# Kernel tuning notes

Measured on AMD Instinct MI355X. Metric: run time of the kernel, lower is better.

Reference implementation:

```python
import jax, jax.numpy as jnp
import numpy as np

N_NODES = 100000


def graph_conv(x, edge_index, w_rel, w_root, b):
    # PyG GraphConv with aggr='add':
    # out_i = W_root @ x_i + W_rel @ (sum_{j in N(i)} x_j) + b
    src, dst = edge_index[0], edge_index[1]
    agg = jax.ops.segment_sum(x[src], dst, num_segments=x.shape[0])  # [N, F_in]
    return x @ w_root.T + agg @ w_rel.T + b


def setup_inputs() -> dict:
    key = jax.random.key(0)
    k = jax.random.split(key, 8)
    c_in, c_hid, c_out = 128, 64, 16
    x = jax.random.normal(k[0], (N_NODES, c_in), dtype=jnp.float32)
    edge_index = jax.random.randint(k[1], (2, 640000), 0, N_NODES, dtype=jnp.int64)
    s1 = 1.0 / np.sqrt(c_in)
    s2 = 1.0 / np.sqrt(c_hid)
    return {
        "x": x,
        "edge_index": edge_index,
        "w1_rel": jax.random.uniform(k[2], (c_hid, c_in), jnp.float32, -s1, s1),
        "w1_root": jax.random.uniform(k[3], (c_hid, c_in), jnp.float32, -s1, s1),
        "b1": jax.random.uniform(k[4], (c_hid,), jnp.float32, -s1, s1),
        "w2_rel": jax.random.uniform(k[5], (c_out, c_hid), jnp.float32, -s2, s2),
        "w2_root": jax.random.uniform(k[6], (c_out, c_hid), jnp.float32, -s2, s2),
        "b2": jax.random.uniform(k[7], (c_out,), jnp.float32, -s2, s2),
    }


def reference(x, edge_index, w1_rel, w1_root, b1, w2_rel, w2_root, b2):
    h = graph_conv(x, edge_index, w1_rel, w1_root, b1)
    h = jax.nn.relu(h)
    # dropout is identity in eval mode (deterministic reference)
    h = graph_conv(h, edge_index, w2_rel, w2_root, b2)
    return jax.nn.log_softmax(h, axis=1)
```

## Files before the change

kernel.cpp:

```cpp
#include <hip/hip_runtime.h>
#include <math.h>

constexpr int CIN = 128, CHID = 64, COUT = 16;

__global__ void detect_kernel(const int* __restrict__ e, int* __restrict__ flag) {
    int v = e[2 * threadIdx.x + 1];
    unsigned long long b = __ballot(v == 0);
    if (threadIdx.x == 0) flag[0] = (b == 0xFFFFFFFFFFFFFFFFULL) ? 1 : 0;
}

__global__ void convert_hist(const int* __restrict__ e, int E,
                             const int* __restrict__ flag,
                             int* __restrict__ srcI, int* __restrict__ dstI,
                             int* __restrict__ counts) {
    int is64 = flag[0];
    int stride = gridDim.x * blockDim.x;
    for (int t = blockIdx.x * blockDim.x + threadIdx.x; t < E; t += stride) {
        int s, d;
        if (is64) { s = e[2 * t]; d = e[2 * (E + t)]; }
        else      { s = e[t];     d = e[E + t];       }
        srcI[t] = s;
        dstI[t] = d;
        atomicAdd(&counts[d], 1);
    }
}

__global__ __launch_bounds__(256)
void scan_partials(const int* __restrict__ counts, int N, int* __restrict__ blocksum) {
    __shared__ int red[256];
    const int tid = threadIdx.x;
    const int base = blockIdx.x * 1024 + tid * 4;
    int s = 0;
#pragma unroll
    for (int i = 0; i < 4; ++i) {
        int idx = base + i;
        if (idx < N) s += counts[idx];
    }
    red[tid] = s;
    __syncthreads();
    for (int d = 128; d > 0; d >>= 1) {
        if (tid < d) red[tid] += red[tid + d];
        __syncthreads();
    }
    if (tid == 0) blocksum[blockIdx.x] = red[0];
}

__global__ __launch_bounds__(1024)
void scan_blocksums(const int* __restrict__ blocksum, int NB, int* __restrict__ blockoff) {
    __shared__ int part[1024];
    const int tid = threadIdx.x;
    part[tid] = (tid < NB) ? blocksum[tid] : 0;
    __syncthreads();
    for (int d = 1; d < 1024; d <<= 1) {
        int v = (tid >= d) ? part[tid - d] : 0;
        __syncthreads();
        part[tid] += v;
        __syncthreads();
    }
    if (tid < NB) blockoff[tid] = (tid == 0) ? 0 : part[tid - 1];
}

__global__ __launch_bounds__(256)
void scan_apply(const int* __restrict__ counts, int N, const int* __restrict__ blockoff,
                int* __restrict__ rowptr, int* __restrict__ cursor) {
    __shared__ int part[256];
    const int tid = threadIdx.x;
    const int base = blockIdx.x * 1024 + tid * 4;
    int c[4];
    int s = 0;
#pragma unroll
    for (int i = 0; i < 4; ++i) {
        int idx = base + i;
        c[i] = (idx < N) ? counts[idx] : 0;
        s += c[i];
    }
    part[tid] = s;
    __syncthreads();
    for (int d = 1; d < 256; d <<= 1) {
        int v = (tid >= d) ? part[tid - d] : 0;
        __syncthreads();
        part[tid] += v;
        __syncthreads();
    }
    int prefix = blockoff[blockIdx.x] + ((tid == 0) ? 0 : part[tid - 1]);
#pragma unroll
    for (int i = 0; i < 4; ++i) {
        int idx = base + i;
        if (idx < N) {
            rowptr[idx] = prefix;
            cursor[idx] = prefix;
            prefix += c[i];
            if (idx == N - 1) rowptr[N] = prefix;
        }
    }
}

__global__ void fill_kernel(const int* __restrict__ srcI, const int* __restrict__ dstI,
                            int E, int* __restrict__ cursor, int* __restrict__ edgesrc) {
    int stride = gridDim.x * blockDim.x;
    for (int t = blockIdx.x * blockDim.x + threadIdx.x; t < E; t += stride) {
        int p = atomicAdd(&cursor[dstI[t]], 1);
        edgesrc[p] = srcI[t];
    }
}

template<int K, int KT, int OH, int NSLOT, int MBLK>
__global__ __launch_bounds__(256)
void gemm_dual48(const float* __restrict__ X, int N,
                 const float* __restrict__ Wa, const float* __restrict__ Wb,
                 const float* __restrict__ bias,
                 float* __restrict__ Da, float* __restrict__ Db) {
    constexpr int O = 2 * OH;
    constexpr int OG = OH / 4;
    constexpr int TILE = NSLOT * MBLK;
    constexpr int BLOCK = OG * NSLOT;
    constexpr int PADKT = KT + 4;
    static_assert(BLOCK == 256, "block size mismatch");

    __shared__ float wT[KT * O];
    __shared__ float xs[TILE * PADKT + (TILE / 8) * 4];
    const int tid = threadIdx.x;

    const int og = tid % OG;
    const int slot = tid / OG;
    const int o4 = og * 4;
    const float4 bv = *(const float4*)&bias[o4];

    const int n0 = blockIdx.x * TILE;
    const int node0 = slot * MBLK;
    const int xbase = node0 * PADKT + (node0 >> 3) * 4;

    float4 accA[MBLK], accB[MBLK];
#pragma unroll
    for (int i = 0; i < MBLK; ++i) {
        accA[i] = make_float4(0.f, 0.f, 0.f, 0.f);
        accB[i] = make_float4(0.f, 0.f, 0.f, 0.f);
    }

    for (int kt = 0; kt < K; kt += KT) {
        for (int i4 = tid; i4 < OH * (KT / 4); i4 += BLOCK) {
            int o = i4 % OH, kq = i4 / OH;
            float4 v = *(const float4*)&Wa[o * K + kt + kq * 4];
            wT[(4 * kq + 0) * O + o] = v.x;
            wT[(4 * kq + 1) * O + o] = v.y;
            wT[(4 * kq + 2) * O + o] = v.z;
            wT[(4 * kq + 3) * O + o] = v.w;
        }
        for (int i4 = tid; i4 < OH * (KT / 4); i4 += BLOCK) {
            int o = i4 % OH, kq = i4 / OH;
            float4 v = *(const float4*)&Wb[o * K + kt + kq * 4];
            wT[(4 * kq + 0) * O + OH + o] = v.x;
            wT[(4 * kq + 1) * O + OH + o] = v.y;
            wT[(4 * kq + 2) * O + OH + o] = v.z;
            wT[(4 * kq + 3) * O + OH + o] = v.w;
        }
        for (int i4 = tid; i4 < TILE * (KT / 4); i4 += BLOCK) {
            int node = i4 / (KT / 4), kq = i4 % (KT / 4);
            int n = n0 + node;
            float4 v = make_float4(0.f, 0.f, 0.f, 0.f);
            if (n < N) v = *(const float4*)&X[(size_t)n * K + kt + kq * 4];
            *(float4*)&xs[node * PADKT + (node >> 3) * 4 + kq * 4] = v;
        }
        __syncthreads();

#pragma unroll 2
        for (int kq = 0; kq < KT / 4; ++kq) {
            const float* wr0 = &wT[(4 * kq + 0) * O];
            const float* wr1 = &wT[(4 * kq + 1) * O];
            const float* wr2 = &wT[(4 * kq + 2) * O];
            const float* wr3 = &wT[(4 * kq + 3) * O];
            float4 wa0 = *(const float4*)&wr0[o4], wb0 = *(const float4*)&wr0[OH + o4];
            float4 wa1 = *(const float4*)&wr1[o4], wb1 = *(const float4*)&wr1[OH + o4];
            float4 wa2 = *(const float4*)&wr2[o4], wb2 = *(const float4*)&wr2[OH + o4];
            float4 wa3 = *(const float4*)&wr3[o4], wb3 = *(const float4*)&wr3[OH + o4];
#pragma unroll
            for (int i = 0; i < MBLK; ++i) {
                float4 xq = *(const float4*)&xs[xbase + i * PADKT + ((node0 + i) >> 3 != node0 >> 3 ? 4 : 0) + kq * 4];
                accA[i].x = fmaf(xq.x, wa0.x, accA[i].x);
                accA[i].y = fmaf(xq.x, wa0.y, accA[i].y);
                accA[i].z = fmaf(xq.x, wa0.z, accA[i].z);
                accA[i].w = fmaf(xq.x, wa0.w, accA[i].w);
                accB[i].x = fmaf(xq.x, wb0.x, accB[i].x);
                accB[i].y = fmaf(xq.x, wb0.y, accB[i].y);
                accB[i].z = fmaf(xq.x, wb0.z, accB[i].z);
                accB[i].w = fmaf(xq.x, wb0.w, accB[i].w);

                accA[i].x = fmaf(xq.y, wa1.x, accA[i].x);
                accA[i].y = fmaf(xq.y, wa1.y, accA[i].y);
                accA[i].z = fmaf(xq.y, wa1.z, accA[i].z);
                accA[i].w = fmaf(xq.y, wa1.w, accA[i].w);
                accB[i].x = fmaf(xq.y, wb1.x, accB[i].x);
                accB[i].y = fmaf(xq.y, wb1.y, accB[i].y);
                accB[i].z = fmaf(xq.y, wb1.z, accB[i].z);
                accB[i].w = fmaf(xq.y, wb1.w, accB[i].w);

                accA[i].x = fmaf(xq.z, wa2.x, accA[i].x);
                accA[i].y = fmaf(xq.z, wa2.y, accA[i].y);
                accA[i].z = fmaf(xq.z, wa2.z, accA[i].z);
                accA[i].w = fmaf(xq.z, wa2.w, accA[i].w);
                accB[i].x = fmaf(xq.z, wb2.x, accB[i].x);
                accB[i].y = fmaf(xq.z, wb2.y, accB[i].y);
                accB[i].z = fmaf(xq.z, wb2.z, accB[i].z);
                accB[i].w = fmaf(xq.z, wb2.w, accB[i].w);

                accA[i].x = fmaf(xq.w, wa3.x, accA[i].x);
                accA[i].y = fmaf(xq.w, wa3.y, accA[i].y);
                accA[i].z = fmaf(xq.w, wa3.z, accA[i].z);
                accA[i].w = fmaf(xq.w, wa3.w, accA[i].w);
                accB[i].x = fmaf(xq.w, wb3.x, accB[i].x);
                accB[i].y = fmaf(xq.w, wb3.y, accB[i].y);
                accB[i].z = fmaf(xq.w, wb3.z, accB[i].z);
                accB[i].w = fmaf(xq.w, wb3.w, accB[i].w);
            }
        }
        __syncthreads();
    }

#pragma unroll
    for (int i = 0; i < MBLK; ++i) {
        int n = n0 + node0 + i;
        if (n >= N) continue;
        float4 ra = accA[i];
        ra.x += bv.x; ra.y += bv.y; ra.z += bv.z; ra.w += bv.w;
        *(float4*)&Da[(size_t)n * OH + o4] = ra;
        *(float4*)&Db[(size_t)n * OH + o4] = accB[i];
    }
}

template<int K, int KT, int OA, int OB, int NSLOT, int T>
__global__ __launch_bounds__(512, 6)
void gemm_dual(const float* __restrict__ X, int N,
               const float* __restrict__ Wa, const float* __restrict__ Wb,
               const float* __restrict__ bias,
               float* __restrict__ Da, float* __restrict__ Db) {
    constexpr int O = OA + OB;
    constexpr int OG = O / 4;
    constexpr int TILE = NSLOT * T;
    constexpr int PADKT = KT + 4;
    constexpr int BLOCK = OG * NSLOT;
    static_assert(BLOCK == 512, "block size mismatch");

    __shared__ float wT[KT * O];
    __shared__ float xs[TILE * PADKT];
    const int tid = threadIdx.x;

    const int og = tid % OG;
    const int slot = tid / OG;
    const int o4 = og * 4;
    float4 bv = make_float4(0.f, 0.f, 0.f, 0.f);
    if (o4 < OA) bv = *(const float4*)&bias[o4];

    const int n0 = blockIdx.x * TILE;

    float4 acc[T];
#pragma unroll
    for (int i = 0; i < T; ++i) acc[i] = make_float4(0.f, 0.f, 0.f, 0.f);

    for (int kt = 0; kt < K; kt += KT) {
        for (int i4 = tid; i4 < OA * (KT / 4); i4 += BLOCK) {
            int o = i4 % OA, kq = i4 / OA;
            float4 v = *(const float4*)&Wa[o * K + kt + kq * 4];
            wT[(4 * kq + 0) * O + o] = v.x;
            wT[(4 * kq + 1) * O + o] = v.y;
            wT[(4 * kq + 2) * O + o] = v.z;
            wT[(4 * kq + 3) * O + o] = v.w;
        }
        for (int i4 = tid; i4 < OB * (KT / 4); i4 += BLOCK) {
            int o = i4 % OB, kq = i4 / OB;
            float4 v = *(const float4*)&Wb[o * K + kt + kq * 4];
            wT[(4 * kq + 0) * O + OA + o] = v.x;
            wT[(4 * kq + 1) * O + OA + o] = v.y;
            wT[(4 * kq + 2) * O + OA + o] = v.z;
            wT[(4 * kq + 3) * O + OA + o] = v.w;
        }
        for (int i4 = tid; i4 < TILE * (KT / 4); i4 += BLOCK) {
            int node = i4 / (KT / 4), kq = i4 % (KT / 4);
            int n = n0 + node;
            float4 v = make_float4(0.f, 0.f, 0.f, 0.f);
            if (n < N) v = *(const float4*)&X[(size_t)n * K + kt + kq * 4];
            *(float4*)&xs[node * PADKT + kq * 4] = v;
        }
        __syncthreads();

        const float* xrow = &xs[slot * T * PADKT];
#pragma unroll 2
        for (int kq = 0; kq < KT / 4; ++kq) {
            float4 w0 = *(const float4*)&wT[(4 * kq + 0) * O + o4];
            float4 w1 = *(const float4*)&wT[(4 * kq + 1) * O + o4];
            float4 w2 = *(const float4*)&wT[(4 * kq + 2) * O + o4];
            float4 w3 = *(const float4*)&wT[(4 * kq + 3) * O + o4];
#pragma unroll
            for (int i = 0; i < T; ++i) {
                float4 xq = *(const float4*)&xrow[i * PADKT + kq * 4];
                acc[i].x = fmaf(xq.x, w0.x, acc[i].x);
                acc[i].y = fmaf(xq.x, w0.y, acc[i].y);
                acc[i].z = fmaf(xq.x, w0.z, acc[i].z);
                acc[i].w = fmaf(xq.x, w0.w, acc[i].w);
                acc[i].x = fmaf(xq.y, w1.x, acc[i].x);
                acc[i].y = fmaf(xq.y, w1.y, acc[i].y);
                acc[i].z = fmaf(xq.y, w1.z, acc[i].z);
                acc[i].w = fmaf(xq.y, w1.w, acc[i].w);
                acc[i].x = fmaf(xq.z, w2.x, acc[i].x);
                acc[i].y = fmaf(xq.z, w2.y, acc[i].y);
                acc[i].z = fmaf(xq.z, w2.z, acc[i].z);
                acc[i].w = fmaf(xq.z, w2.w, acc[i].w);
                acc[i].x = fmaf(xq.w, w3.x, acc[i].x);
                acc[i].y = fmaf(xq.w, w3.y, acc[i].y);
                acc[i].z = fmaf(xq.w, w3.z, acc[i].z);
                acc[i].w = fmaf(xq.w, w3.w, acc[i].w);
            }
        }
        __syncthreads();
    }

#pragma unroll
    for (int i = 0; i < T; ++i) {
        int n = n0 + slot * T + i;
        if (n >= N) continue;
        float4 r = acc[i];
        if (o4 < OA) {
            r.x += bv.x; r.y += bv.y; r.z += bv.z; r.w += bv.w;
            *(float4*)&Da[(size_t)n * OA + o4] = r;
        } else {
            *(float4*)&Db[(size_t)n * OB + (o4 - OA)] = r;
        }
    }
}

__global__ void gather_relu64(const int* __restrict__ rowptr, const int* __restrict__ edgesrc,
                              const float* __restrict__ T1, float* __restrict__ A, int N) {
    constexpr int F = 64, Q = F / 4;
    int idx = blockIdx.x * blockDim.x + threadIdx.x;
    int n = idx / Q, q = idx % Q;
    if (n >= N) return;
    int beg = rowptr[n], end = rowptr[n + 1];
    float4 acc0 = make_float4(0.f, 0.f, 0.f, 0.f);
    float4 acc1 = make_float4(0.f, 0.f, 0.f, 0.f);
    int j = beg;
    for (; j + 1 < end; j += 2) {
        int s0 = edgesrc[j];
        int s1 = edgesrc[j + 1];
        float4 v0 = *(const float4*)&T1[(size_t)s0 * F + q * 4];
        float4 v1 = *(const float4*)&T1[(size_t)s1 * F + q * 4];
        acc0.x += v0.x; acc0.y += v0.y; acc0.z += v0.z; acc0.w += v0.w;
        acc1.x += v1.x; acc1.y += v1.y; acc1.z += v1.z; acc1.w += v1.w;
    }
    if (j < end) {
        int s0 = edgesrc[j];
        float4 v0 = *(const float4*)&T1[(size_t)s0 * F + q * 4];
        acc0.x += v0.x; acc0.y += v0.y; acc0.z += v0.z; acc0.w += v0.w;
    }
    acc0.x += acc1.x; acc0.y += acc1.y; acc0.z += acc1.z; acc0.w += acc1.w;
    float4 a = *(const float4*)&A[(size_t)n * F + q * 4];
    a.x = fmaxf(a.x + acc0.x, 0.f);
    a.y = fmaxf(a.y + acc0.y, 0.f);
    a.z = fmaxf(a.z + acc0.z, 0.f);
    a.w = fmaxf(a.w + acc0.w, 0.f);
    *(float4*)&A[(size_t)n * F + q * 4] = a;
}

__global__ void gather_lsm(const int* __restrict__ rowptr, const int* __restrict__ edgesrc,
                           const float* __restrict__ T3, const float* __restrict__ T2,
                           float* __restrict__ out, int N) {
    int idx = blockIdx.x * blockDim.x + threadIdx.x;
    int n = idx / 4, c = idx % 4;
    if (n >= N) return;
    int beg = rowptr[n], end = rowptr[n + 1];
    float4 acc0 = make_float4(0.f, 0.f, 0.f, 0.f);
    float4 acc1 = make_float4(0.f, 0.f, 0.f, 0.f);
    int j = beg;
    for (; j + 1 < end; j += 2) {
        int s0 = edgesrc[j];
        int s1 = edgesrc[j + 1];
        float4 v0 = *(const float4*)&T2[(size_t)s0 * 16 + c * 4];
        float4 v1 = *(const float4*)&T2[(size_t)s1 * 16 + c * 4];
        acc0.x += v0.x; acc0.y += v0.y; acc0.z += v0.z; acc0.w += v0.w;
        acc1.x += v1.x; acc1.y += v1.y; acc1.z += v1.z; acc1.w += v1.w;
    }
    if (j < end) {
        int s0 = edgesrc[j];
        float4 v0 = *(const float4*)&T2[(size_t)s0 * 16 + c * 4];
        acc0.x += v0.x; acc0.y += v0.y; acc0.z += v0.z; acc0.w += v0.w;
    }
    acc0.x += acc1.x; acc0.y += acc1.y; acc0.z += acc1.z; acc0.w += acc1.w;
    float4 t = *(const float4*)&T3[(size_t)n * 16 + c * 4];
    float4 v = make_float4(t.x + acc0.x, t.y + acc0.y, t.z + acc0.z, t.w + acc0.w);
    float m = fmaxf(fmaxf(v.x, v.y), fmaxf(v.z, v.w));
    for (int d = 1; d < 4; d <<= 1) m = fmaxf(m, __shfl_xor(m, d, 4));
    float s = expf(v.x - m) + expf(v.y - m) + expf(v.z - m) + expf(v.w - m);
    for (int d = 1; d < 4; d <<= 1) s += __shfl_xor(s, d, 4);
    float ls = m + logf(s);
    float4 r = make_float4(v.x - ls, v.y - ls, v.z - ls, v.w - ls);
    *(float4*)&out[(size_t)n * 16 + c * 4] = r;
}

extern "C" void kernel_launch(void* const* d_in, const int* in_sizes, int n_in,
                              void* d_out, int out_size, void* d_ws, size_t ws_size,
                              hipStream_t stream) {
    const float* X      = (const float*)d_in[0];
    const int*   EIDX   = (const int*)d_in[1];
    const float* W1REL  = (const float*)d_in[2];
    const float* W1ROOT = (const float*)d_in[3];
    const float* B1     = (const float*)d_in[4];
    const float* W2REL  = (const float*)d_in[5];
    const float* W2ROOT = (const float*)d_in[6];
    const float* B2     = (const float*)d_in[7];
    float* OUT = (float*)d_out;

    const int N = in_sizes[0] / CIN;
    const int E = in_sizes[1] / 2;
    const int NB = (N + 1023) / 1024;

    char* wsb = (char*)d_ws;
    size_t off = 0;
    auto alloc = [&](size_t bytes) { void* p = wsb + off; off += (bytes + 255) & ~size_t(255); return p; };

    int* flag     = (int*)alloc(256);
    int* srcI     = (int*)alloc((size_t)E * 4);
    int* dstI     = (int*)alloc((size_t)E * 4);
    int* edgesrc  = (int*)alloc((size_t)E * 4);
    int* counts   = (int*)alloc((size_t)N * 4);
    int* rowptr   = (int*)alloc((size_t)(N + 1) * 4);
    int* cursor   = (int*)alloc((size_t)N * 4);
    int* blocksum = (int*)alloc((size_t)NB * 4);
    int* blockoff = (int*)alloc((size_t)NB * 4);
    float* A      = (float*)alloc((size_t)N * CHID * 4);
    float* Bt     = (float*)alloc((size_t)N * CHID * 4);
    if (off > ws_size) return;

    float* T3 = Bt;
    float* T2 = Bt + (size_t)N * COUT;

    hipMemsetAsync(counts, 0, (size_t)N * 4, stream);

    detect_kernel<<<1, 64, 0, stream>>>(EIDX, flag);
    convert_hist<<<1024, 256, 0, stream>>>(EIDX, E, flag, srcI, dstI, counts);
    scan_partials<<<NB, 256, 0, stream>>>(counts, N, blocksum);
    scan_blocksums<<<1, 1024, 0, stream>>>(blocksum, NB, blockoff);
    scan_apply<<<NB, 256, 0, stream>>>(counts, N, blockoff, rowptr, cursor);
    fill_kernel<<<1024, 256, 0, stream>>>(srcI, dstI, E, cursor, edgesrc);

    {
        constexpr int TILE = 16 * 4;
        int grid = (N + TILE - 1) / TILE;
        gemm_dual48<128, 32, 64, 16, 4><<<grid, 256, 0, stream>>>(X, N, W1ROOT, W1REL, B1, A, Bt);
    }

    {
        int threads = N * 16;
        gather_relu64<<<(threads + 255) / 256, 256, 0, stream>>>(rowptr, edgesrc, Bt, A, N);
    }

    {
        constexpr int TILE = 64 * 2;
        int grid = (N + TILE - 1) / TILE;
        gemm_dual<64, 32, 16, 16, 64, 2><<<grid, 512, 0, stream>>>(A, N, W2ROOT, W2REL, B2, T3, T2);
    }

    {
        int threads = N * 4;
        gather_lsm<<<(threads + 255) / 256, 256, 0, stream>>>(rowptr, edgesrc, T3, T2, OUT, N);
    }
}
```

Baseline: 194.2 us.

## Fuse layer-1 gather+ReLU into layer-2 dual GEMM via shared-memory tile

Removes the separate gather_relu64 kernel. The layer-2 GEMM now gathers neighbor sums from Bt, adds the root term and applies ReLU directly into its shared-memory input tile, so the hidden activations are never written back to A and re-read. Weights are loaded once with the full K=64, which removes the K-tiling loop and one barrier per tile. T3 and T2 get their own buffers because Bt is still being read during the fused kernel. The irregular gather now runs inside a 512-thread block before a barrier, so load imbalance between nodes could leave the FMA phase waiting.

```diff
diff --git a/kernel.cpp b/kernel.cpp
--- a/kernel.cpp
+++ b/kernel.cpp
@@ -227,21 +227,23 @@
     }
 }
 
-template<int K, int KT, int OA, int OB, int NSLOT, int T>
-__global__ __launch_bounds__(512, 6)
-void gemm_dual(const float* __restrict__ X, int N,
-               const float* __restrict__ Wa, const float* __restrict__ Wb,
-               const float* __restrict__ bias,
-               float* __restrict__ Da, float* __restrict__ Db) {
+template<int K, int OA, int OB, int NSLOT, int T>
+__global__ __launch_bounds__(512)
+void gemm2_fused(const float* __restrict__ T0, const float* __restrict__ T1, int N,
+                 const int* __restrict__ rowptr, const int* __restrict__ edgesrc,
+                 const float* __restrict__ Wa, const float* __restrict__ Wb,
+                 const float* __restrict__ bias,
+                 float* __restrict__ Da, float* __restrict__ Db) {
     constexpr int O = OA + OB;
     constexpr int OG = O / 4;
     constexpr int TILE = NSLOT * T;
-    constexpr int PADKT = KT + 4;
+    constexpr int PADK = K + 4;
     constexpr int BLOCK = OG * NSLOT;
     static_assert(BLOCK == 512, "block size mismatch");
-
-    __shared__ float wT[KT * O];
-    __shared__ float xs[TILE * PADKT];
+    static_assert(K == CHID, "single-pass K");
+
+    __shared__ float wT[K * O];
+    __shared__ float xs[TILE * PADK];
     const int tid = threadIdx.x;
 
     const int og = tid % OG;
@@ -252,65 +254,89 @@
 
     const int n0 = blockIdx.x * TILE;
 
+    for (int i4 = tid; i4 < OA * (K / 4); i4 += BLOCK) {
+        int o = i4 % OA, kq = i4 / OA;
+        float4 v = *(const float4*)&Wa[o * K + kq * 4];
+        wT[(4 * kq + 0) * O + o] = v.x;
+        wT[(4 * kq + 1) * O + o] = v.y;
+        wT[(4 * kq + 2) * O + o] = v.z;
+        wT[(4 * kq + 3) * O + o] = v.w;
+    }
+    for (int i4 = tid; i4 < OB * (K / 4); i4 += BLOCK) {
+        int o = i4 % OB, kq = i4 / OB;
+        float4 v = *(const float4*)&Wb[o * K + kq * 4];
+        wT[(4 * kq + 0) * O + OA + o] = v.x;
+        wT[(4 * kq + 1) * O + OA + o] = v.y;
+        wT[(4 * kq + 2) * O + OA + o] = v.z;
+        wT[(4 * kq + 3) * O + OA + o] = v.w;
+    }
+
+    {
+        const int g = tid >> 4;
+        const int q = tid & 15;
+        for (int node = g; node < TILE; node += 32) {
+            int n = n0 + node;
+            float4 h = make_float4(0.f, 0.f, 0.f, 0.f);
+            if (n < N) {
+                int beg = rowptr[n], end = rowptr[n + 1];
+                float4 a0 = make_float4(0.f, 0.f, 0.f, 0.f);
+                float4 a1 = make_float4(0.f, 0.f, 0.f, 0.f);
+                int j = beg;
+                for (; j + 1 < end; j += 2) {
+                    int s0 = edgesrc[j];
+                    int s1 = edgesrc[j + 1];
+                    float4 v0 = *(const float4*)&T1[(size_t)s0 * K + q * 4];
+                    float4 v1 = *(const float4*)&T1[(size_t)s1 * K + q * 4];
+                    a0.x += v0.x; a0.y += v0.y; a0.z += v0.z; a0.w += v0.w;
+                    a1.x += v1.x; a1.y += v1.y; a1.z += v1.z; a1.w += v1.w;
+                }
+                if (j < end) {
+                    int s0 = edgesrc[j];
+                    float4 v0 = *(const float4*)&T1[(size_t)s0 * K + q * 4];
+                    a0.x += v0.x; a0.y += v0.y; a0.z += v0.z; a0.w += v0.w;
+                }
+                float4 t = *(const float4*)&T0[(size_t)n * K + q * 4];
+                h.x = fmaxf(t.x + a0.x + a1.x, 0.f);
+                h.y = fmaxf(t.y + a0.y + a1.y, 0.f);
+                h.z = fmaxf(t.z + a0.z + a1.z, 0.f);
+                h.w = fmaxf(t.w + a0.w + a1.w, 0.f);
+            }
+            *(float4*)&xs[node * PADK + q * 4] = h;
+        }
+    }
+    __syncthreads();
+
     float4 acc[T];
 #pragma unroll
     for (int i = 0; i < T; ++i) acc[i] = make_float4(0.f, 0.f, 0.f, 0.f);
 
-    for (int kt = 0; kt < K; kt += KT) {
-        for (int i4 = tid; i4 < OA * (KT / 4); i4 += BLOCK) {
-            int o = i4 % OA, kq = i4 / OA;
-            float4 v = *(const float4*)&Wa[o * K + kt + kq * 4];
-            wT[(4 * kq + 0) * O + o] = v.x;
-            wT[(4 * kq + 1) * O + o] = v.y;
-            wT[(4 * kq + 2) * O + o] = v.z;
-            wT[(4 * kq + 3) * O + o] = v.w;
-        }
-        for (int i4 = tid; i4 < OB * (KT / 4); i4 += BLOCK) {
-            int o = i4 % OB, kq = i4 / OB;
-            float4 v = *(const float4*)&Wb[o * K + kt + kq * 4];
-            wT[(4 * kq + 0) * O + OA + o] = v.x;
-            wT[(4 * kq + 1) * O + OA + o] = v.y;
-            wT[(4 * kq + 2) * O + OA + o] = v.z;
-            wT[(4 * kq + 3) * O + OA + o] = v.w;
-        }
-        for (int i4 = tid; i4 < TILE * (KT / 4); i4 += BLOCK) {
-            int node = i4 / (KT / 4), kq = i4 % (KT / 4);
-            int n = n0 + node;
-            float4 v = make_float4(0.f, 0.f, 0.f, 0.f);
-            if (n < N) v = *(const float4*)&X[(size_t)n * K + kt + kq * 4];
-            *(float4*)&xs[node * PADKT + kq * 4] = v;
-        }
-        __syncthreads();
-
-        const float* xrow = &xs[slot * T * PADKT];
+    const float* xrow = &xs[slot * T * PADK];
 #pragma unroll 2
-        for (int kq = 0; kq < KT / 4; ++kq) {
-            float4 w0 = *(const float4*)&wT[(4 * kq + 0) * O + o4];
-            float4 w1 = *(const float4*)&wT[(4 * kq + 1) * O + o4];
-            float4 w2 = *(const float4*)&wT[(4 * kq + 2) * O + o4];
-            float4 w3 = *(const float4*)&wT[(4 * kq + 3) * O + o4];
-#pragma unroll
-            for (int i = 0; i < T; ++i) {
-                float4 xq = *(const float4*)&xrow[i * PADKT + kq * 4];
-                acc[i].x = fmaf(xq.x, w0.x, acc[i].x);
-                acc[i].y = fmaf(xq.x, w0.y, acc[i].y);
-                acc[i].z = fmaf(xq.x, w0.z, acc[i].z);
-                acc[i].w = fmaf(xq.x, w0.w, acc[i].w);
-                acc[i].x = fmaf(xq.y, w1.x, acc[i].x);
-                acc[i].y = fmaf(xq.y, w1.y, acc[i].y);
-                acc[i].z = fmaf(xq.y, w1.z, acc[i].z);
-                acc[i].w = fmaf(xq.y, w1.w, acc[i].w);
-                acc[i].x = fmaf(xq.z, w2.x, acc[i].x);
-                acc[i].y = fmaf(xq.z, w2.y, acc[i].y);
-                acc[i].z = fmaf(xq.z, w2.z, acc[i].z);
-                acc[i].w = fmaf(xq.z, w2.w, acc[i].w);
-                acc[i].x = fmaf(xq.w, w3.x, acc[i].x);
-                acc[i].y = fmaf(xq.w, w3.y, acc[i].y);
-                acc[i].z = fmaf(xq.w, w3.z, acc[i].z);
-                acc[i].w = fmaf(xq.w, w3.w, acc[i].w);
-            }
-        }
-        __syncthreads();
+    for (int kq = 0; kq < K / 4; ++kq) {
+        float4 w0 = *(const float4*)&wT[(4 * kq + 0) * O + o4];
+        float4 w1 = *(const float4*)&wT[(4 * kq + 1) * O + o4];
+        float4 w2 = *(const float4*)&wT[(4 * kq + 2) * O + o4];
+        float4 w3 = *(const float4*)&wT[(4 * kq + 3) * O + o4];
+#pragma unroll
+        for (int i = 0; i < T; ++i) {
+            float4 xq = *(const float4*)&xrow[i * PADK + kq * 4];
+            acc[i].x = fmaf(xq.x, w0.x, acc[i].x);
+            acc[i].y = fmaf(xq.x, w0.y, acc[i].y);
+            acc[i].z = fmaf(xq.x, w0.z, acc[i].z);
+            acc[i].w = fmaf(xq.x, w0.w, acc[i].w);
+            acc[i].x = fmaf(xq.y, w1.x, acc[i].x);
+            acc[i].y = fmaf(xq.y, w1.y, acc[i].y);
+            acc[i].z = fmaf(xq.y, w1.z, acc[i].z);
+            acc[i].w = fmaf(xq.y, w1.w, acc[i].w);
+            acc[i].x = fmaf(xq.z, w2.x, acc[i].x);
+            acc[i].y = fmaf(xq.z, w2.y, acc[i].y);
+            acc[i].z = fmaf(xq.z, w2.z, acc[i].z);
+            acc[i].w = fmaf(xq.z, w2.w, acc[i].w);
+            acc[i].x = fmaf(xq.w, w3.x, acc[i].x);
+            acc[i].y = fmaf(xq.w, w3.y, acc[i].y);
+            acc[i].z = fmaf(xq.w, w3.z, acc[i].z);
+            acc[i].w = fmaf(xq.w, w3.w, acc[i].w);
+        }
     }
 
 #pragma unroll
@@ -325,38 +351,6 @@
             *(float4*)&Db[(size_t)n * OB + (o4 - OA)] = r;
         }
     }
-}
-
-__global__ void gather_relu64(const int* __restrict__ rowptr, const int* __restrict__ edgesrc,
-                              const float* __restrict__ T1, float* __restrict__ A, int N) {
-    constexpr int F = 64, Q = F / 4;
-    int idx = blockIdx.x * blockDim.x + threadIdx.x;
-    int n = idx / Q, q = idx % Q;
-    if (n >= N) return;
-    int beg = rowptr[n], end = rowptr[n + 1];
-    float4 acc0 = make_float4(0.f, 0.f, 0.f, 0.f);
-    float4 acc1 = make_float4(0.f, 0.f, 0.f, 0.f);
-    int j = beg;
-    for (; j + 1 < end; j += 2) {
-        int s0 = edgesrc[j];
-        int s1 = edgesrc[j + 1];
-        float4 v0 = *(const float4*)&T1[(size_t)s0 * F + q * 4];
-        float4 v1 = *(const float4*)&T1[(size_t)s1 * F + q * 4];
-        acc0.x += v0.x; acc0.y += v0.y; acc0.z += v0.z; acc0.w += v0.w;
-        acc1.x += v1.x; acc1.y += v1.y; acc1.z += v1.z; acc1.w += v1.w;
-    }
-    if (j < end) {
-        int s0 = edgesrc[j];
-        float4 v0 = *(const float4*)&T1[(size_t)s0 * F + q * 4];
-        acc0.x += v0.x; acc0.y += v0.y; acc0.z += v0.z; acc0.w += v0.w;
-    }
-    acc0.x += acc1.x; acc0.y += acc1.y; acc0.z += acc1.z; acc0.w += acc1.w;
-    float4 a = *(const float4*)&A[(size_t)n * F + q * 4];
-    a.x = fmaxf(a.x + acc0.x, 0.f);
-    a.y = fmaxf(a.y + acc0.y, 0.f);
-    a.z = fmaxf(a.z + acc0.z, 0.f);
-    a.w = fmaxf(a.w + acc0.w, 0.f);
-    *(float4*)&A[(size_t)n * F + q * 4] = a;
 }
 
 __global__ void gather_lsm(const int* __restrict__ rowptr, const int* __restrict__ edgesrc,
@@ -426,10 +420,9 @@
     int* blockoff = (int*)alloc((size_t)NB * 4);
     float* A      = (float*)alloc((size_t)N * CHID * 4);
     float* Bt     = (float*)alloc((size_t)N * CHID * 4);
+    float* T3     = (float*)alloc((size_t)N * COUT * 4);
+    float* T2     = (float*)alloc((size_t)N * COUT * 4);
     if (off > ws_size) return;
-
-    float* T3 = Bt;
-    float* T2 = Bt + (size_t)N * COUT;
 
     hipMemsetAsync(counts, 0, (size_t)N * 4, stream);
 
@@ -447,14 +440,10 @@
     }
 
     {
-        int threads = N * 16;
-        gather_relu64<<<(threads + 255) / 256, 256, 0, stream>>>(rowptr, edgesrc, Bt, A, N);
-    }
-
-    {
         constexpr int TILE = 64 * 2;
         int grid = (N + TILE - 1) / TILE;
-        gemm_dual<64, 32, 16, 16, 64, 2><<<grid, 512, 0, stream>>>(A, N, W2ROOT, W2REL, B2, T3, T2);
+        gemm2_fused<64, 16, 16, 64, 2><<<grid, 512, 0, stream>>>(
+            A, Bt, N, rowptr, edgesrc, W2ROOT, W2REL, B2, T3, T2);
     }
 
     {
```

Result: slower. 202.4 us (+4.2%).
